# Kernel tuning notes

Measured on AMD Instinct MI355X. Metric: run time of the kernel, lower is better.

## Reference

```python
import jax, jax.numpy as jnp
import numpy as np

NU, NI, D, E = 50000, 100000, 128, 500000
UMAX, IMAX = 50, 50
SQRT_D = float(np.sqrt(D))


def seg_softmax(vals, seg, n):
    # numerically stable softmax over edges grouped by segment id (sparse row softmax)
    m = jax.ops.segment_max(vals, seg, num_segments=n)
    ex = jnp.exp(vals - m[seg])
    s = jax.ops.segment_sum(ex, seg, num_segments=n)
    return ex / s[seg]


def setup_inputs() -> dict:
    key = jax.random.key(0)
    ks = jax.random.split(key, 20)
    w = lambda k: jax.random.normal(k, (D, D), dtype=jnp.float32) * 0.05
    return {
        "u_emb": jax.random.normal(ks[0], (NU, D), dtype=jnp.float32),
        "i_emb": jax.random.normal(ks[1], (NI, D), dtype=jnp.float32),
        "edge_u": jax.random.randint(ks[2], (E,), 0, NU),
        "edge_i": jax.random.randint(ks[3], (E,), 0, NI),
        "rui": jax.random.randint(ks[4], (E,), 0, UMAX),
        "riu": jax.random.randint(ks[5], (E,), 0, IMAX),
        "last_u_items": jax.random.randint(ks[6], (NU,), 0, NI),
        "last_i_users": jax.random.randint(ks[7], (NU,), 0, NU),
        "W1": w(ks[8]), "W2": w(ks[9]), "W1b": w(ks[10]), "W2b": w(ks[11]),
        "W3": w(ks[12]), "W4": w(ks[13]),
        "pV": jax.random.normal(ks[14], (UMAX, D), dtype=jnp.float32),
        "pK": jax.random.normal(ks[15], (IMAX, D), dtype=jnp.float32),
        "last_user_table": jax.random.normal(ks[16], (NU, D), dtype=jnp.float32),
        "last_item_table": jax.random.normal(ks[17], (NI, D), dtype=jnp.float32),
    }


def reference(u_emb, i_emb, edge_u, edge_i, rui, riu, last_u_items, last_i_users,
              W1, W2, W1b, W2b, W3, W4, pV, pK, last_user_table, last_item_table):
    # nn.Linear: y = x @ W.T
    um = u_emb @ W2.T            # (NU, D) user messages
    im = i_emb @ W1.T            # (NI, D) item messages
    um_e = um[edge_u]            # (E, D) gathered per edge
    im_e = im[edge_i]            # (E, D)

    # ---- long term ----
    # dense e = um @ im.T masked to edges == per-edge dot products (same math)
    e_vals = jnp.sum(um_e * im_e, axis=-1)                     # (E,)
    pVui = pV[rui]                                             # (E, D)
    pKiu = pK[riu]                                             # (E, D)
    e_ui = e_vals + jnp.sum(um_e * pVui, axis=-1)
    e_iu = e_vals + jnp.sum(im_e * pKiu, axis=-1)
    alphas = seg_softmax(e_ui / SQRT_D, edge_u, NU)            # softmax over items per user
    betas = seg_softmax(e_iu / SQRT_D, edge_i, NI)             # softmax over users per item

    umb = u_emb @ W2b.T
    imb = i_emb @ W1b.T
    # pass_messages: out[row] = sum_e alpha_e * (messages[col_e] + p_e)
    hLu = jax.ops.segment_sum(alphas[:, None] * (imb[edge_i] + pKiu), edge_u, num_segments=NU)
    hLi = jax.ops.segment_sum(betas[:, None] * (umb[edge_u] + pVui), edge_i, num_segments=NI)

    # ---- short term ----
    li = last_item_table[last_u_items] @ W3.T                  # (NU, D)
    lu = last_user_table[last_i_users] @ W4.T                  # (NU, D)
    a_vals = jnp.sum(li[edge_u] * im_e, axis=-1)               # (E,)
    b_vals = jnp.sum(lu[edge_u] * im_e, axis=-1)               # (E,)
    alphas_s = seg_softmax(a_vals / SQRT_D, edge_u, NU)
    betas_s = seg_softmax(b_vals / SQRT_D, edge_i, NI)
    # p = ones -> messages + 1
    hSu = jax.ops.segment_sum(alphas_s[:, None] * (im_e + 1.0), edge_u, num_segments=NU)
    hSi = jax.ops.segment_sum(betas_s[:, None] * (um_e + 1.0), edge_i, num_segments=NI)

    return (hLu, hSu, hLi, hSi)
```

## Files before the change

kernel.cpp:

```cpp
#include <hip/hip_runtime.h>
#include <hip/hip_bf16.h>
#include <math.h>

#define D_ 128
#define INV_SQRT_D 0.08838834764831845f
#define SCAN_CH 16
#define SCAN_TILE (256 * SCAN_CH)

typedef __bf16 bf16x8 __attribute__((ext_vector_type(8)));
typedef float f32x4 __attribute__((ext_vector_type(4)));

struct W6 { const float* p[6]; };

__device__ __forceinline__ void unpack8(bf16x8 v, float* f) {
    const uint32_t* u = (const uint32_t*)&v;
#pragma unroll
    for (int i = 0; i < 4; i++) {
        uint32_t w = u[i];
        f[2 * i]     = __uint_as_float(w << 16);
        f[2 * i + 1] = __uint_as_float(w & 0xffff0000u);
    }
}

__global__ __launch_bounds__(256) void cvt_weights(W6 w, __bf16* __restrict__ out) {
    int idx = blockIdx.x * 256 + threadIdx.x;
    if (idx >= 6 * 16384) return;
    out[idx] = (__bf16)w.p[idx >> 14][idx & 16383];
}

__global__ __launch_bounds__(256) void cvt2(const float* __restrict__ a, const float* __restrict__ b,
                                            __bf16* __restrict__ oa, __bf16* __restrict__ ob, int n) {
    int idx = blockIdx.x * 256 + threadIdx.x;
    if (idx < n) { oa[idx] = (__bf16)a[idx]; ob[idx] = (__bf16)b[idx]; }
}

__global__ __launch_bounds__(256) void gemm_dual(const float* __restrict__ X,
                                                 const __bf16* __restrict__ WA,
                                                 const __bf16* __restrict__ WB,
                                                 __bf16* __restrict__ YA, int sA,
                                                 __bf16* __restrict__ YB, int sB, int rows) {
    int lane = threadIdx.x & 63;
    int wave = threadIdx.x >> 6;
    int row0 = blockIdx.x * 64 + wave * 16;
    if (row0 >= rows) return;
    int l16 = lane & 15, kh = lane >> 4;
    int ar = row0 + l16;
    int arc = ar < rows ? ar : rows - 1;
    const float* arow = X + (size_t)arc * D_;

    f32x4 accA[8] = {}, accB[8] = {};
#pragma unroll
    for (int k0 = 0; k0 < D_; k0 += 32) {
        int kk = k0 + kh * 8;
        float4 a0 = *(const float4*)(arow + kk);
        float4 a1 = *(const float4*)(arow + kk + 4);
        bf16x8 af;
        af[0] = (__bf16)a0.x; af[1] = (__bf16)a0.y; af[2] = (__bf16)a0.z; af[3] = (__bf16)a0.w;
        af[4] = (__bf16)a1.x; af[5] = (__bf16)a1.y; af[6] = (__bf16)a1.z; af[7] = (__bf16)a1.w;
#pragma unroll
        for (int cb = 0; cb < 8; cb++) {
            bf16x8 bfA = *(const bf16x8*)(WA + (size_t)(cb * 16 + l16) * D_ + kk);
            accA[cb] = __builtin_amdgcn_mfma_f32_16x16x32_bf16(af, bfA, accA[cb], 0, 0, 0);
            bf16x8 bfB = *(const bf16x8*)(WB + (size_t)(cb * 16 + l16) * D_ + kk);
            accB[cb] = __builtin_amdgcn_mfma_f32_16x16x32_bf16(af, bfB, accB[cb], 0, 0, 0);
        }
    }
#pragma unroll
    for (int cb = 0; cb < 8; cb++) {
#pragma unroll
        for (int j = 0; j < 4; j++) {
            int r = row0 + kh * 4 + j;
            if (r < rows) {
                YA[(size_t)r * sA + cb * 16 + l16] = (__bf16)accA[cb][j];
                YB[(size_t)r * sB + cb * 16 + l16] = (__bf16)accB[cb][j];
            }
        }
    }
}

__global__ __launch_bounds__(256) void gemm_lilu(const float* __restrict__ Xi, const int* __restrict__ gi_,
                                                 const float* __restrict__ Xu, const int* __restrict__ gu_,
                                                 const __bf16* __restrict__ Wli, const __bf16* __restrict__ Wlu,
                                                 __bf16* __restrict__ Yli, __bf16* __restrict__ Ylu, int rows) {
    int lane = threadIdx.x & 63;
    int wave = threadIdx.x >> 6;
    int row0 = blockIdx.x * 64 + wave * 16;
    if (row0 >= rows) return;
    int l16 = lane & 15, kh = lane >> 4;
    int ar = row0 + l16;
    int arc = ar < rows ? ar : rows - 1;
    const float* arowA = Xi + (size_t)gi_[arc] * D_;
    const float* arowB = Xu + (size_t)gu_[arc] * D_;

    f32x4 accA[8] = {}, accB[8] = {};
#pragma unroll
    for (int k0 = 0; k0 < D_; k0 += 32) {
        int kk = k0 + kh * 8;
        float4 a0 = *(const float4*)(arowA + kk);
        float4 a1 = *(const float4*)(arowA + kk + 4);
        float4 b0 = *(const float4*)(arowB + kk);
        float4 b1 = *(const float4*)(arowB + kk + 4);
        bf16x8 afA, afB;
        afA[0] = (__bf16)a0.x; afA[1] = (__bf16)a0.y; afA[2] = (__bf16)a0.z; afA[3] = (__bf16)a0.w;
        afA[4] = (__bf16)a1.x; afA[5] = (__bf16)a1.y; afA[6] = (__bf16)a1.z; afA[7] = (__bf16)a1.w;
        afB[0] = (__bf16)b0.x; afB[1] = (__bf16)b0.y; afB[2] = (__bf16)b0.z; afB[3] = (__bf16)b0.w;
        afB[4] = (__bf16)b1.x; afB[5] = (__bf16)b1.y; afB[6] = (__bf16)b1.z; afB[7] = (__bf16)b1.w;
#pragma unroll
        for (int cb = 0; cb < 8; cb++) {
            bf16x8 bfA = *(const bf16x8*)(Wli + (size_t)(cb * 16 + l16) * D_ + kk);
            accA[cb] = __builtin_amdgcn_mfma_f32_16x16x32_bf16(afA, bfA, accA[cb], 0, 0, 0);
            bf16x8 bfB = *(const bf16x8*)(Wlu + (size_t)(cb * 16 + l16) * D_ + kk);
            accB[cb] = __builtin_amdgcn_mfma_f32_16x16x32_bf16(afB, bfB, accB[cb], 0, 0, 0);
        }
    }
#pragma unroll
    for (int cb = 0; cb < 8; cb++) {
#pragma unroll
        for (int j = 0; j < 4; j++) {
            int r = row0 + kh * 4 + j;
            if (r < rows) {
                Yli[(size_t)r * D_ + cb * 16 + l16] = (__bf16)accA[cb][j];
                Ylu[(size_t)r * D_ + cb * 16 + l16] = (__bf16)accB[cb][j];
            }
        }
    }
}

__global__ __launch_bounds__(256) void gemm_pvk(const __bf16* __restrict__ Xb, int xstride,
                                                const __bf16* __restrict__ Pb,
                                                float* __restrict__ Y, int rows, int ncols) {
    int lane = threadIdx.x & 63;
    int wave = threadIdx.x >> 6;
    int row0 = blockIdx.x * 64 + wave * 16;
    if (row0 >= rows) return;
    int l16 = lane & 15, kh = lane >> 4;
    int ar = row0 + l16;
    int arc = ar < rows ? ar : rows - 1;
    const __bf16* arow = Xb + (size_t)arc * xstride;

    f32x4 acc[4] = {};
#pragma unroll
    for (int k0 = 0; k0 < D_; k0 += 32) {
        int kk = k0 + kh * 8;
        bf16x8 af = *(const bf16x8*)(arow + kk);
#pragma unroll
        for (int cb = 0; cb < 4; cb++) {
            int br = cb * 16 + l16;
            if (br >= ncols) br = ncols - 1;
            bf16x8 bf = *(const bf16x8*)(Pb + (size_t)br * D_ + kk);
            acc[cb] = __builtin_amdgcn_mfma_f32_16x16x32_bf16(af, bf, acc[cb], 0, 0, 0);
        }
    }
#pragma unroll
    for (int cb = 0; cb < 4; cb++) {
        int col = cb * 16 + l16;
        if (col >= ncols) continue;
#pragma unroll
        for (int j = 0; j < 4; j++) {
            int r = row0 + kh * 4 + j;
            if (r < rows) Y[(size_t)r * ncols + col] = acc[cb][j] * INV_SQRT_D;
        }
    }
}

__global__ __launch_bounds__(256) void hist2(const int* __restrict__ eu, const int* __restrict__ ei,
                                             int* __restrict__ cnt_all, int nu, int E) {
    int e = blockIdx.x * 256 + threadIdx.x;
    if (e < E) {
        atomicAdd(&cnt_all[eu[e]], 1);
        atomicAdd(&cnt_all[nu + ei[e]], 1);
    }
}

__global__ __launch_bounds__(256) void scan_phaseA(const int* __restrict__ cnt, int* __restrict__ part, int n) {
    __shared__ int wsum[4];
    int t = threadIdx.x, lane = t & 63, w = t >> 6;
    int i0 = blockIdx.x * SCAN_TILE + t * SCAN_CH;
    int tot = 0;
#pragma unroll
    for (int j = 0; j < SCAN_CH; j++) tot += (i0 + j < n) ? cnt[i0 + j] : 0;
#pragma unroll
    for (int d = 32; d; d >>= 1) tot += __shfl_xor(tot, d);
    if (lane == 0) wsum[w] = tot;
    __syncthreads();
    if (t == 0) part[blockIdx.x] = wsum[0] + wsum[1] + wsum[2] + wsum[3];
}

__global__ __launch_bounds__(1024) void scan_phaseB(int* __restrict__ part, int nb,
                                                    int* __restrict__ off, int n) {
    __shared__ int wsum[16];
    int t = threadIdx.x, lane = t & 63, w = t >> 6;
    int v = (t < nb) ? part[t] : 0;
    int x = v;
#pragma unroll
    for (int d = 1; d < 64; d <<= 1) {
        int y = __shfl_up(x, d);
        if (lane >= d) x += y;
    }
    if (lane == 63) wsum[w] = x;
    __syncthreads();
    int wbase = 0;
    for (int ww = 0; ww < w; ww++) wbase += wsum[ww];
    if (t < nb) part[t] = wbase + x - v;
    if (t == 1023) off[n] = wbase + x;
}

__global__ __launch_bounds__(256) void scan_phaseC(const int* __restrict__ cnt, const int* __restrict__ part,
                                                   int* __restrict__ off, int* __restrict__ pos, int n) {
    __shared__ int wsum[4];
    int t = threadIdx.x, lane = t & 63, w = t >> 6;
    int i0 = blockIdx.x * SCAN_TILE + t * SCAN_CH;
    int loc[SCAN_CH];
    int tot = 0;
#pragma unroll
    for (int j = 0; j < SCAN_CH; j++) {
        int v = (i0 + j < n) ? cnt[i0 + j] : 0;
        loc[j] = tot; tot += v;
    }
    int x = tot;
#pragma unroll
    for (int d = 1; d < 64; d <<= 1) {
        int y = __shfl_up(x, d);
        if (lane >= d) x += y;
    }
    if (lane == 63) wsum[w] = x;
    __syncthreads();
    int wbase = 0;
    for (int ww = 0; ww < w; ww++) wbase += wsum[ww];
    int excl = part[blockIdx.x] + wbase + x - tot;
#pragma unroll
    for (int j = 0; j < SCAN_CH; j++) {
        if (i0 + j < n) { off[i0 + j] = excl + loc[j]; pos[i0 + j] = excl + loc[j]; }
    }
}

__global__ __launch_bounds__(256) void scatter2(const int* __restrict__ eu, const int* __restrict__ ei,
                                                const int* __restrict__ rui, const int* __restrict__ riu,
                                                int* __restrict__ pos_all, int4* __restrict__ recs,
                                                int nu, int E) {
    int e = blockIdx.x * 256 + threadIdx.x;
    if (e < E) {
        int u = eu[e], it = ei[e], r1 = rui[e], r2 = riu[e];
        int pi = atomicAdd(&pos_all[nu + it], 1);
        int pu = atomicAdd(&pos_all[u], 1);
        recs[pu] = make_int4(it, r1, r2, pi);
        recs[pi] = make_int4(u, r1, r2, 0);
    }
}

__global__ __launch_bounds__(256) void user_fused(const int* __restrict__ off_all, const int4* __restrict__ recs,
                                                  const __bf16* __restrict__ i_rec,
                                                  const __bf16* __restrict__ u_rec,
                                                  const __bf16* __restrict__ li_t,
                                                  const __bf16* __restrict__ lu_t,
                                                  const __bf16* __restrict__ pKb,
                                                  const float* __restrict__ upv,
                                                  float2* __restrict__ mb_val,
                                                  float* __restrict__ hLu, float* __restrict__ hSu,
                                                  int nu, int umax) {
    int u = blockIdx.x * 4 + (threadIdx.x >> 6);
    if (u >= nu) return;
    int lane = threadIdx.x & 63;
    int g = lane >> 4, l16 = lane & 15;
    int off = off_all[u], n = off_all[u + 1] - off;
    if (n == 0) {
        if (lane < 16) {
            float4 z = make_float4(0.f, 0.f, 0.f, 0.f);
            ((float4*)(hLu + (size_t)u * D_ + l16 * 8))[0] = z;
            ((float4*)(hLu + (size_t)u * D_ + l16 * 8))[1] = z;
            ((float4*)(hSu + (size_t)u * D_ + l16 * 8))[0] = z;
            ((float4*)(hSu + (size_t)u * D_ + l16 * 8))[1] = z;
        }
        return;
    }
    float um8[8], li8[8], lu8[8];
    unpack8(((const bf16x8*)(u_rec + (size_t)u * 256))[l16], um8);
    unpack8(((const bf16x8*)(li_t + (size_t)u * D_))[l16], li8);
    unpack8(((const bf16x8*)(lu_t + (size_t)u * D_))[l16], lu8);
#pragma unroll
    for (int j = 0; j < 8; j++) { um8[j] *= INV_SQRT_D; li8[j] *= INV_SQRT_D; lu8[j] *= INV_SQRT_D; }
    const float* upv_row = upv + (size_t)u * umax;

    float s1 = 0.f, s2 = 0.f, a1[8] = {}, a2[8] = {};
    for (int i = g; i < n; i += 8) {
        int4 ra = recs[off + i];
        bool hb = (i + 4) < n;
        int4 rb = recs[off + (hb ? i + 4 : i)];
        const __bf16* pa = i_rec + (size_t)ra.x * 256;
        const __bf16* pb = i_rec + (size_t)rb.x * 256;
        bf16x8 vimA = ((const bf16x8*)pa)[l16];
        bf16x8 vmbA = ((const bf16x8*)(pa + 128))[l16];
        bf16x8 vpkA = ((const bf16x8*)(pKb + (size_t)ra.z * D_))[l16];
        bf16x8 vimB = ((const bf16x8*)pb)[l16];
        bf16x8 vmbB = ((const bf16x8*)(pb + 128))[l16];
        bf16x8 vpkB = ((const bf16x8*)(pKb + (size_t)rb.z * D_))[l16];
        float fimA[8], fmbA[8], fpkA[8], fimB[8], fmbB[8], fpkB[8];
        unpack8(vimA, fimA); unpack8(vmbA, fmbA); unpack8(vpkA, fpkA);
        unpack8(vimB, fimB); unpack8(vmbB, fmbB); unpack8(vpkB, fpkB);
        float d1a = 0.f, d2a = 0.f, d3a = 0.f, d1b = 0.f, d2b = 0.f, d3b = 0.f;
#pragma unroll
        for (int j = 0; j < 8; j++) {
            d1a = fmaf(um8[j], fimA[j], d1a);
            d2a = fmaf(li8[j], fimA[j], d2a);
            d3a = fmaf(lu8[j], fimA[j], d3a);
            d1b = fmaf(um8[j], fimB[j], d1b);
            d2b = fmaf(li8[j], fimB[j], d2b);
            d3b = fmaf(lu8[j], fimB[j], d3b);
        }
#pragma unroll
        for (int d = 1; d < 16; d <<= 1) {
            d1a += __shfl_xor(d1a, d); d2a += __shfl_xor(d2a, d); d3a += __shfl_xor(d3a, d);
            d1b += __shfl_xor(d1b, d); d2b += __shfl_xor(d2b, d); d3b += __shfl_xor(d3b, d);
        }
        if (l16 == 0) {
            mb_val[ra.w] = make_float2(d1a, d3a);
            if (hb) mb_val[rb.w] = make_float2(d1b, d3b);
        }
        float w1a = __expf(d1a + upv_row[ra.y]);
        float w2a = __expf(d2a);
        float w1b = hb ? __expf(d1b + upv_row[rb.y]) : 0.f;
        float w2b = hb ? __expf(d2b) : 0.f;
        s1 += w1a + w1b; s2 += w2a + w2b;
#pragma unroll
        for (int j = 0; j < 8; j++) {
            a1[j] = fmaf(w1a, fmbA[j] + fpkA[j], fmaf(w1b, fmbB[j] + fpkB[j], a1[j]));
            a2[j] = fmaf(w2a, fimA[j], fmaf(w2b, fimB[j], a2[j]));
        }
    }
#pragma unroll
    for (int d = 16; d < 64; d <<= 1) {
        s1 += __shfl_xor(s1, d); s2 += __shfl_xor(s2, d);
#pragma unroll
        for (int j = 0; j < 8; j++) {
            a1[j] += __shfl_xor(a1[j], d);
            a2[j] += __shfl_xor(a2[j], d);
        }
    }
    if (lane < 16) {
        float inv1 = 1.f / s1, inv2 = 1.f / s2;
        ((float4*)(hLu + (size_t)u * D_ + l16 * 8))[0] = make_float4(a1[0]*inv1, a1[1]*inv1, a1[2]*inv1, a1[3]*inv1);
        ((float4*)(hLu + (size_t)u * D_ + l16 * 8))[1] = make_float4(a1[4]*inv1, a1[5]*inv1, a1[6]*inv1, a1[7]*inv1);
        ((float4*)(hSu + (size_t)u * D_ + l16 * 8))[0] = make_float4(a2[0]*inv2+1.f, a2[1]*inv2+1.f, a2[2]*inv2+1.f, a2[3]*inv2+1.f);
        ((float4*)(hSu + (size_t)u * D_ + l16 * 8))[1] = make_float4(a2[4]*inv2+1.f, a2[5]*inv2+1.f, a2[6]*inv2+1.f, a2[7]*inv2+1.f);
    }
}

__global__ __launch_bounds__(256) void item_fused(const int* __restrict__ off_all, const int4* __restrict__ recs,
                                                  const __bf16* __restrict__ u_rec,
                                                  const __bf16* __restrict__ pVb,
                                                  const float* __restrict__ ipk,
                                                  const float2* __restrict__ mb_val,
                                                  float* __restrict__ hLi, float* __restrict__ hSi,
                                                  int nu, int ni, int imax) {
    int it = blockIdx.x * 4 + (threadIdx.x >> 6);
    if (it >= ni) return;
    int lane = threadIdx.x & 63;
    int g = lane >> 4, l16 = lane & 15;
    int off = off_all[nu + it], n = off_all[nu + it + 1] - off;
    if (n == 0) {
        if (lane < 16) {
            float4 z = make_float4(0.f, 0.f, 0.f, 0.f);
            ((float4*)(hLi + (size_t)it * D_ + l16 * 8))[0] = z;
            ((float4*)(hLi + (size_t)it * D_ + l16 * 8))[1] = z;
            ((float4*)(hSi + (size_t)it * D_ + l16 * 8))[0] = z;
            ((float4*)(hSi + (size_t)it * D_ + l16 * 8))[1] = z;
        }
        return;
    }
    const float* ipk_row = ipk + (size_t)it * imax;

    float s1 = 0.f, s2 = 0.f, a1[8] = {}, a2[8] = {};
    for (int i = g; i < n; i += 8) {
        int4 ra = recs[off + i];
        bool hb = (i + 4) < n;
        int4 rb = recs[off + (hb ? i + 4 : i)];
        float2 ma = mb_val[off + i];
        float2 mbv = hb ? mb_val[off + i + 4] : make_float2(0.f, 0.f);
        const __bf16* pa = u_rec + (size_t)ra.x * 256;
        const __bf16* pb = u_rec + (size_t)rb.x * 256;
        bf16x8 vumA  = ((const bf16x8*)pa)[l16];
        bf16x8 vmbA  = ((const bf16x8*)(pa + 128))[l16];
        bf16x8 vpvA  = ((const bf16x8*)(pVb + (size_t)ra.y * D_))[l16];
        bf16x8 vumB  = ((const bf16x8*)pb)[l16];
        bf16x8 vmbB  = ((const bf16x8*)(pb + 128))[l16];
        bf16x8 vpvB  = ((const bf16x8*)(pVb + (size_t)rb.y * D_))[l16];
        float fumA[8], fmbA[8], fpvA[8], fumB[8], fmbB[8], fpvB[8];
        unpack8(vumA, fumA); unpack8(vmbA, fmbA); unpack8(vpvA, fpvA);
        unpack8(vumB, fumB); unpack8(vmbB, fmbB); unpack8(vpvB, fpvB);
        float w1a = __expf(ma.x + ipk_row[ra.z]);
        float w2a = __expf(ma.y);
        float w1b = hb ? __expf(mbv.x + ipk_row[rb.z]) : 0.f;
        float w2b = hb ? __expf(mbv.y) : 0.f;
        s1 += w1a + w1b; s2 += w2a + w2b;
#pragma unroll
        for (int j = 0; j < 8; j++) {
            a1[j] = fmaf(w1a, fmbA[j] + fpvA[j], fmaf(w1b, fmbB[j] + fpvB[j], a1[j]));
            a2[j] = fmaf(w2a, fumA[j], fmaf(w2b, fumB[j], a2[j]));
        }
    }
#pragma unroll
    for (int d = 16; d < 64; d <<= 1) {
        s1 += __shfl_xor(s1, d); s2 += __shfl_xor(s2, d);
#pragma unroll
        for (int j = 0; j < 8; j++) {
            a1[j] += __shfl_xor(a1[j], d);
            a2[j] += __shfl_xor(a2[j], d);
        }
    }
    if (lane < 16) {
        float inv1 = 1.f / s1, inv2 = 1.f / s2;
        ((float4*)(hLi + (size_t)it * D_ + l16 * 8))[0] = make_float4(a1[0]*inv1, a1[1]*inv1, a1[2]*inv1, a1[3]*inv1);
        ((float4*)(hLi + (size_t)it * D_ + l16 * 8))[1] = make_float4(a1[4]*inv1, a1[5]*inv1, a1[6]*inv1, a1[7]*inv1);
        ((float4*)(hSi + (size_t)it * D_ + l16 * 8))[0] = make_float4(a2[0]*inv2+1.f, a2[1]*inv2+1.f, a2[2]*inv2+1.f, a2[3]*inv2+1.f);
        ((float4*)(hSi + (size_t)it * D_ + l16 * 8))[1] = make_float4(a2[4]*inv2+1.f, a2[5]*inv2+1.f, a2[6]*inv2+1.f, a2[7]*inv2+1.f);
    }
}

extern "C" void kernel_launch(void* const* d_in, const int* in_sizes, int n_in,
                              void* d_out, int out_size, void* d_ws, size_t ws_size,
                              hipStream_t stream) {
    (void)n_in; (void)out_size; (void)ws_size;
    const float* u_emb = (const float*)d_in[0];
    const float* i_emb = (const float*)d_in[1];
    const int* edge_u = (const int*)d_in[2];
    const int* edge_i = (const int*)d_in[3];
    const int* rui = (const int*)d_in[4];
    const int* riu = (const int*)d_in[5];
    const int* last_u_items = (const int*)d_in[6];
    const int* last_i_users = (const int*)d_in[7];
    const float* W1  = (const float*)d_in[8];
    const float* W2  = (const float*)d_in[9];
    const float* W1b = (const float*)d_in[10];
    const float* W2b = (const float*)d_in[11];
    const float* W3  = (const float*)d_in[12];
    const float* W4  = (const float*)d_in[13];
    const float* pV  = (const float*)d_in[14];
    const float* pK  = (const float*)d_in[15];
    const float* last_user_table = (const float*)d_in[16];
    const float* last_item_table = (const float*)d_in[17];

    const int NU = in_sizes[0] / D_;
    const int NI = in_sizes[1] / D_;
    const int E  = in_sizes[2];
    const int UMAXr = in_sizes[14] / D_;
    const int IMAXr = in_sizes[15] / D_;
    const int NSEG = NU + NI;

    size_t cur = 0;
    auto alloc = [&](size_t bytes) -> void* {
        void* p = (char*)d_ws + cur;
        cur += (bytes + 255) & ~(size_t)255;
        return p;
    };

    __bf16* Wb    = (__bf16*)alloc(6 * 16384 * sizeof(__bf16));
    __bf16* pVb   = (__bf16*)alloc((size_t)UMAXr * D_ * 2);
    __bf16* pKb   = (__bf16*)alloc((size_t)IMAXr * D_ * 2);
    __bf16* i_rec = (__bf16*)alloc((size_t)NI * 256 * 2);
    __bf16* u_rec = (__bf16*)alloc((size_t)NU * 256 * 2);
    __bf16* li_bf = (__bf16*)alloc((size_t)NU * D_ * 2);
    __bf16* lu_bf = (__bf16*)alloc((size_t)NU * D_ * 2);
    float* upv    = (float*)alloc((size_t)NU * UMAXr * 4);
    float* ipk    = (float*)alloc((size_t)NI * IMAXr * 4);
    float2* mb_val = (float2*)alloc((size_t)2 * E * 8);
    int4* recs    = (int4*)alloc((size_t)2 * E * 16);
    int* cnt_all  = (int*)alloc((size_t)NSEG * 4);
    int* off_all  = (int*)alloc((size_t)(NSEG + 1) * 4);
    int* pos_all  = (int*)alloc((size_t)NSEG * 4);
    int* parts    = (int*)alloc(1024 * 4);

    float* out = (float*)d_out;
    float* hLu = out;
    float* hSu = out + (size_t)NU * D_;
    float* hLi = out + (size_t)2 * NU * D_;
    float* hSi = out + (size_t)2 * NU * D_ + (size_t)NI * D_;

    W6 w6;
    w6.p[0] = W1; w6.p[1] = W2; w6.p[2] = W1b; w6.p[3] = W2b; w6.p[4] = W3; w6.p[5] = W4;
    cvt_weights<<<(6 * 16384 + 255) / 256, 256, 0, stream>>>(w6, Wb);
    cvt2<<<(UMAXr * D_ + 255) / 256, 256, 0, stream>>>(pV, pK, pVb, pKb, UMAXr * D_);

    hipMemsetAsync(cnt_all, 0, (size_t)NSEG * 4, stream);
    hist2<<<(E + 255) / 256, 256, 0, stream>>>(edge_u, edge_i, cnt_all, NU, E);
    int nb = (NSEG + SCAN_TILE - 1) / SCAN_TILE;
    scan_phaseA<<<nb, 256, 0, stream>>>(cnt_all, parts, NSEG);
    scan_phaseB<<<1, 1024, 0, stream>>>(parts, nb, off_all, NSEG);
    scan_phaseC<<<nb, 256, 0, stream>>>(cnt_all, parts, off_all, pos_all, NSEG);
    scatter2<<<(E + 255) / 256, 256, 0, stream>>>(edge_u, edge_i, rui, riu, pos_all, recs, NU, E);

    int gu = (NU + 63) / 64, gi = (NI + 63) / 64;
    gemm_dual<<<gi, 256, 0, stream>>>(i_emb, Wb + 0 * 16384, Wb + 2 * 16384,
                                      i_rec + 0, 256, i_rec + 128, 256, NI);
    gemm_dual<<<gu, 256, 0, stream>>>(u_emb, Wb + 1 * 16384, Wb + 3 * 16384,
                                      u_rec + 0, 256, u_rec + 128, 256, NU);
    gemm_lilu<<<gu, 256, 0, stream>>>(last_item_table, last_u_items, last_user_table, last_i_users,
                                      Wb + 4 * 16384, Wb + 5 * 16384, li_bf, lu_bf, NU);

    gemm_pvk<<<gu, 256, 0, stream>>>(u_rec, 256, pVb, upv, NU, UMAXr);
    gemm_pvk<<<gi, 256, 0, stream>>>(i_rec, 256, pKb, ipk, NI, IMAXr);

    user_fused<<<(NU + 3) / 4, 256, 0, stream>>>(off_all, recs, i_rec, u_rec, li_bf, lu_bf,
                                                 pKb, upv, mb_val, hLu, hSu, NU, UMAXr);
    item_fused<<<(NI + 3) / 4, 256, 0, stream>>>(off_all, recs, u_rec, pVb, ipk, mb_val,
                                                 hLi, hSi, NU, NI, IMAXr);
}
```

Before: 489.3 us.

## Reassociate projections: gather raw bf16 embeddings, apply weights after aggregation

Folds the weight matrices algebraically. Combined matrices such as W1ᵀW2, W1ᵀW3, W1ᵀW4 and pV·W2 are precomputed so that per-edge scores use raw bf16 embeddings instead of projected messages. The segment aggregation now runs on raw embeddings, and the W1b/W2b and W1/W2 projections are applied once per node afterwards in a new finish GEMM, which also adds the positional term and the +1 offset. This halves the bytes gathered per edge (128 instead of 256 bf16 per record) and removes the item/user message GEMMs before the passes. In exchange it adds an embedding conversion pass, bf16 intermediate buffers and two post-GEMMs, and changes where rounding happens.

```diff
diff --git a/kernel.cpp b/kernel.cpp
--- a/kernel.cpp
+++ b/kernel.cpp
@@ -10,7 +10,7 @@
 typedef __bf16 bf16x8 __attribute__((ext_vector_type(8)));
 typedef float f32x4 __attribute__((ext_vector_type(4)));
 
-struct W6 { const float* p[6]; };
+struct W4p { const float* p[4]; };
 
 __device__ __forceinline__ void unpack8(bf16x8 v, float* f) {
     const uint32_t* u = (const uint32_t*)&v;
@@ -22,9 +22,16 @@
     }
 }
 
-__global__ __launch_bounds__(256) void cvt_weights(W6 w, __bf16* __restrict__ out) {
+__device__ __forceinline__ bf16x8 pack8(const float* f, float s) {
+    bf16x8 r;
+#pragma unroll
+    for (int j = 0; j < 8; j++) r[j] = (__bf16)(f[j] * s);
+    return r;
+}
+
+__global__ __launch_bounds__(256) void cvt_weights4(W4p w, __bf16* __restrict__ out) {
     int idx = blockIdx.x * 256 + threadIdx.x;
-    if (idx >= 6 * 16384) return;
+    if (idx >= 4 * 16384) return;
     out[idx] = (__bf16)w.p[idx >> 14][idx & 16383];
 }
 
@@ -34,11 +41,64 @@
     if (idx < n) { oa[idx] = (__bf16)a[idx]; ob[idx] = (__bf16)b[idx]; }
 }
 
-__global__ __launch_bounds__(256) void gemm_dual(const float* __restrict__ X,
-                                                 const __bf16* __restrict__ WA,
-                                                 const __bf16* __restrict__ WB,
-                                                 __bf16* __restrict__ YA, int sA,
-                                                 __bf16* __restrict__ YB, int sB, int rows) {
+__global__ __launch_bounds__(256) void cvt_emb(const float* __restrict__ u, const float* __restrict__ i,
+                                               __bf16* __restrict__ ub, __bf16* __restrict__ ib,
+                                               size_t nue, size_t nie) {
+    size_t idx4 = ((size_t)blockIdx.x * 256 + threadIdx.x) * 4;
+    if (idx4 < nue) {
+        float4 v = *(const float4*)(u + idx4);
+        ub[idx4] = (__bf16)v.x; ub[idx4+1] = (__bf16)v.y; ub[idx4+2] = (__bf16)v.z; ub[idx4+3] = (__bf16)v.w;
+    } else if (idx4 < nue + nie) {
+        size_t j = idx4 - nue;
+        float4 v = *(const float4*)(i + j);
+        ib[j] = (__bf16)v.x; ib[j+1] = (__bf16)v.y; ib[j+2] = (__bf16)v.z; ib[j+3] = (__bf16)v.w;
+    }
+}
+
+__global__ __launch_bounds__(128) void prep_mats(const float* __restrict__ W1, const float* __restrict__ W2,
+                                                 const float* __restrict__ W3, const float* __restrict__ W4,
+                                                 const float* __restrict__ pV, const float* __restrict__ pK,
+                                                 __bf16* __restrict__ M2t, __bf16* __restrict__ M3t,
+                                                 __bf16* __restrict__ M4t,
+                                                 __bf16* __restrict__ pVW2, __bf16* __restrict__ pKW1,
+                                                 int umax, int imax) {
+    __shared__ float sh[256];
+    int b = blockIdx.x, t = threadIdx.x;
+    if (b < 128) {
+        sh[t] = W1[t * 128 + b];
+        __syncthreads();
+        float m2 = 0.f, m3 = 0.f, m4 = 0.f;
+        for (int k = 0; k < 128; k++) {
+            float w = sh[k];
+            m2 = fmaf(w, W2[k * 128 + t], m2);
+            m3 = fmaf(w, W3[k * 128 + t], m3);
+            m4 = fmaf(w, W4[k * 128 + t], m4);
+        }
+        M2t[b * 128 + t] = (__bf16)(m2 * INV_SQRT_D);
+        M3t[b * 128 + t] = (__bf16)(m3 * INV_SQRT_D);
+        M4t[b * 128 + t] = (__bf16)(m4 * INV_SQRT_D);
+    } else {
+        int r = b - 128;
+        if (r < umax) sh[t] = pV[r * 128 + t];
+        if (r < imax) sh[128 + t] = pK[r * 128 + t];
+        __syncthreads();
+        float q = 0.f, qk = 0.f;
+        for (int a = 0; a < 128; a++) {
+            if (r < umax) q  = fmaf(sh[a], W2[a * 128 + t], q);
+            if (r < imax) qk = fmaf(sh[128 + a], W1[a * 128 + t], qk);
+        }
+        if (r < umax) pVW2[r * 128 + t] = (__bf16)(q * INV_SQRT_D);
+        if (r < imax) pKW1[r * 128 + t] = (__bf16)(qk * INV_SQRT_D);
+    }
+}
+
+__global__ __launch_bounds__(256) void user_vecs(const float* __restrict__ u_emb,
+                                                 const float* __restrict__ lit_tab, const int* __restrict__ g_li,
+                                                 const float* __restrict__ lut_tab, const int* __restrict__ g_lu,
+                                                 const __bf16* __restrict__ M2t, const __bf16* __restrict__ M3t,
+                                                 const __bf16* __restrict__ M4t,
+                                                 __bf16* __restrict__ um_t, __bf16* __restrict__ li_t,
+                                                 __bf16* __restrict__ lu_t, int rows) {
     int lane = threadIdx.x & 63;
     int wave = threadIdx.x >> 6;
     int row0 = blockIdx.x * 64 + wave * 16;
@@ -46,23 +106,32 @@
     int l16 = lane & 15, kh = lane >> 4;
     int ar = row0 + l16;
     int arc = ar < rows ? ar : rows - 1;
-    const float* arow = X + (size_t)arc * D_;
-
-    f32x4 accA[8] = {}, accB[8] = {};
+    const float* rA = u_emb + (size_t)arc * D_;
+    const float* rB = lit_tab + (size_t)g_li[arc] * D_;
+    const float* rC = lut_tab + (size_t)g_lu[arc] * D_;
+
+    f32x4 aA[8] = {}, aB[8] = {}, aC[8] = {};
 #pragma unroll
     for (int k0 = 0; k0 < D_; k0 += 32) {
         int kk = k0 + kh * 8;
-        float4 a0 = *(const float4*)(arow + kk);
-        float4 a1 = *(const float4*)(arow + kk + 4);
-        bf16x8 af;
-        af[0] = (__bf16)a0.x; af[1] = (__bf16)a0.y; af[2] = (__bf16)a0.z; af[3] = (__bf16)a0.w;
-        af[4] = (__bf16)a1.x; af[5] = (__bf16)a1.y; af[6] = (__bf16)a1.z; af[7] = (__bf16)a1.w;
+        float4 a0 = *(const float4*)(rA + kk), a1 = *(const float4*)(rA + kk + 4);
+        float4 b0 = *(const float4*)(rB + kk), b1 = *(const float4*)(rB + kk + 4);
+        float4 c0 = *(const float4*)(rC + kk), c1 = *(const float4*)(rC + kk + 4);
+        bf16x8 fA, fB, fC;
+        fA[0]=(__bf16)a0.x; fA[1]=(__bf16)a0.y; fA[2]=(__bf16)a0.z; fA[3]=(__bf16)a0.w;
+        fA[4]=(__bf16)a1.x; fA[5]=(__bf16)a1.y; fA[6]=(__bf16)a1.z; fA[7]=(__bf16)a1.w;
+        fB[0]=(__bf16)b0.x; fB[1]=(__bf16)b0.y; fB[2]=(__bf16)b0.z; fB[3]=(__bf16)b0.w;
+        fB[4]=(__bf16)b1.x; fB[5]=(__bf16)b1.y; fB[6]=(__bf16)b1.z; fB[7]=(__bf16)b1.w;
+        fC[0]=(__bf16)c0.x; fC[1]=(__bf16)c0.y; fC[2]=(__bf16)c0.z; fC[3]=(__bf16)c0.w;
+        fC[4]=(__bf16)c1.x; fC[5]=(__bf16)c1.y; fC[6]=(__bf16)c1.z; fC[7]=(__bf16)c1.w;
 #pragma unroll
         for (int cb = 0; cb < 8; cb++) {
-            bf16x8 bfA = *(const bf16x8*)(WA + (size_t)(cb * 16 + l16) * D_ + kk);
-            accA[cb] = __builtin_amdgcn_mfma_f32_16x16x32_bf16(af, bfA, accA[cb], 0, 0, 0);
-            bf16x8 bfB = *(const bf16x8*)(WB + (size_t)(cb * 16 + l16) * D_ + kk);
-            accB[cb] = __builtin_amdgcn_mfma_f32_16x16x32_bf16(af, bfB, accB[cb], 0, 0, 0);
+            bf16x8 w2 = *(const bf16x8*)(M2t + (size_t)(cb * 16 + l16) * D_ + kk);
+            aA[cb] = __builtin_amdgcn_mfma_f32_16x16x32_bf16(fA, w2, aA[cb], 0, 0, 0);
+            bf16x8 w3 = *(const bf16x8*)(M3t + (size_t)(cb * 16 + l16) * D_ + kk);
+            aB[cb] = __builtin_amdgcn_mfma_f32_16x16x32_bf16(fB, w3, aB[cb], 0, 0, 0);
+            bf16x8 w4 = *(const bf16x8*)(M4t + (size_t)(cb * 16 + l16) * D_ + kk);
+            aC[cb] = __builtin_amdgcn_mfma_f32_16x16x32_bf16(fC, w4, aC[cb], 0, 0, 0);
         }
     }
 #pragma unroll
@@ -71,62 +140,15 @@
         for (int j = 0; j < 4; j++) {
             int r = row0 + kh * 4 + j;
             if (r < rows) {
-                YA[(size_t)r * sA + cb * 16 + l16] = (__bf16)accA[cb][j];
-                YB[(size_t)r * sB + cb * 16 + l16] = (__bf16)accB[cb][j];
+                um_t[(size_t)r * D_ + cb * 16 + l16] = (__bf16)aA[cb][j];
+                li_t[(size_t)r * D_ + cb * 16 + l16] = (__bf16)aB[cb][j];
+                lu_t[(size_t)r * D_ + cb * 16 + l16] = (__bf16)aC[cb][j];
             }
         }
     }
 }
 
-__global__ __launch_bounds__(256) void gemm_lilu(const float* __restrict__ Xi, const int* __restrict__ gi_,
-                                                 const float* __restrict__ Xu, const int* __restrict__ gu_,
-                                                 const __bf16* __restrict__ Wli, const __bf16* __restrict__ Wlu,
-                                                 __bf16* __restrict__ Yli, __bf16* __restrict__ Ylu, int rows) {
-    int lane = threadIdx.x & 63;
-    int wave = threadIdx.x >> 6;
-    int row0 = blockIdx.x * 64 + wave * 16;
-    if (row0 >= rows) return;
-    int l16 = lane & 15, kh = lane >> 4;
-    int ar = row0 + l16;
-    int arc = ar < rows ? ar : rows - 1;
-    const float* arowA = Xi + (size_t)gi_[arc] * D_;
-    const float* arowB = Xu + (size_t)gu_[arc] * D_;
-
-    f32x4 accA[8] = {}, accB[8] = {};
-#pragma unroll
-    for (int k0 = 0; k0 < D_; k0 += 32) {
-        int kk = k0 + kh * 8;
-        float4 a0 = *(const float4*)(arowA + kk);
-        float4 a1 = *(const float4*)(arowA + kk + 4);
-        float4 b0 = *(const float4*)(arowB + kk);
-        float4 b1 = *(const float4*)(arowB + kk + 4);
-        bf16x8 afA, afB;
-        afA[0] = (__bf16)a0.x; afA[1] = (__bf16)a0.y; afA[2] = (__bf16)a0.z; afA[3] = (__bf16)a0.w;
-        afA[4] = (__bf16)a1.x; afA[5] = (__bf16)a1.y; afA[6] = (__bf16)a1.z; afA[7] = (__bf16)a1.w;
-        afB[0] = (__bf16)b0.x; afB[1] = (__bf16)b0.y; afB[2] = (__bf16)b0.z; afB[3] = (__bf16)b0.w;
-        afB[4] = (__bf16)b1.x; afB[5] = (__bf16)b1.y; afB[6] = (__bf16)b1.z; afB[7] = (__bf16)b1.w;
-#pragma unroll
-        for (int cb = 0; cb < 8; cb++) {
-            bf16x8 bfA = *(const bf16x8*)(Wli + (size_t)(cb * 16 + l16) * D_ + kk);
-            accA[cb] = __builtin_amdgcn_mfma_f32_16x16x32_bf16(afA, bfA, accA[cb], 0, 0, 0);
-            bf16x8 bfB = *(const bf16x8*)(Wlu + (size_t)(cb * 16 + l16) * D_ + kk);
-            accB[cb] = __builtin_amdgcn_mfma_f32_16x16x32_bf16(afB, bfB, accB[cb], 0, 0, 0);
-        }
-    }
-#pragma unroll
-    for (int cb = 0; cb < 8; cb++) {
-#pragma unroll
-        for (int j = 0; j < 4; j++) {
-            int r = row0 + kh * 4 + j;
-            if (r < rows) {
-                Yli[(size_t)r * D_ + cb * 16 + l16] = (__bf16)accA[cb][j];
-                Ylu[(size_t)r * D_ + cb * 16 + l16] = (__bf16)accB[cb][j];
-            }
-        }
-    }
-}
-
-__global__ __launch_bounds__(256) void gemm_pvk(const __bf16* __restrict__ Xb, int xstride,
+__global__ __launch_bounds__(256) void gemm_pvk(const __bf16* __restrict__ Xb,
                                                 const __bf16* __restrict__ Pb,
                                                 float* __restrict__ Y, int rows, int ncols) {
     int lane = threadIdx.x & 63;
@@ -136,7 +158,7 @@
     int l16 = lane & 15, kh = lane >> 4;
     int ar = row0 + l16;
     int arc = ar < rows ? ar : rows - 1;
-    const __bf16* arow = Xb + (size_t)arc * xstride;
+    const __bf16* arow = Xb + (size_t)arc * D_;
 
     f32x4 acc[4] = {};
 #pragma unroll
@@ -158,7 +180,7 @@
 #pragma unroll
         for (int j = 0; j < 4; j++) {
             int r = row0 + kh * 4 + j;
-            if (r < rows) Y[(size_t)r * ncols + col] = acc[cb][j] * INV_SQRT_D;
+            if (r < rows) Y[(size_t)r * ncols + col] = acc[cb][j];
         }
     }
 }
@@ -248,16 +270,16 @@
     }
 }
 
-__global__ __launch_bounds__(256) void user_fused(const int* __restrict__ off_all, const int4* __restrict__ recs,
-                                                  const __bf16* __restrict__ i_rec,
-                                                  const __bf16* __restrict__ u_rec,
-                                                  const __bf16* __restrict__ li_t,
-                                                  const __bf16* __restrict__ lu_t,
-                                                  const __bf16* __restrict__ pKb,
-                                                  const float* __restrict__ upv,
-                                                  float2* __restrict__ mb_val,
-                                                  float* __restrict__ hLu, float* __restrict__ hSu,
-                                                  int nu, int umax) {
+__global__ __launch_bounds__(256) void user_pass(const int* __restrict__ off_all, const int4* __restrict__ recs,
+                                                 const __bf16* __restrict__ ib_emb,
+                                                 const __bf16* __restrict__ um_t,
+                                                 const __bf16* __restrict__ li_t,
+                                                 const __bf16* __restrict__ lu_t,
+                                                 const __bf16* __restrict__ pKb,
+                                                 const float* __restrict__ upv,
+                                                 float2* __restrict__ mb_val,
+                                                 __bf16* __restrict__ A1n, __bf16* __restrict__ PKn,
+                                                 __bf16* __restrict__ A2n, int nu, int umax) {
     int u = blockIdx.x * 4 + (threadIdx.x >> 6);
     if (u >= nu) return;
     int lane = threadIdx.x & 63;
@@ -265,47 +287,40 @@
     int off = off_all[u], n = off_all[u + 1] - off;
     if (n == 0) {
         if (lane < 16) {
-            float4 z = make_float4(0.f, 0.f, 0.f, 0.f);
-            ((float4*)(hLu + (size_t)u * D_ + l16 * 8))[0] = z;
-            ((float4*)(hLu + (size_t)u * D_ + l16 * 8))[1] = z;
-            ((float4*)(hSu + (size_t)u * D_ + l16 * 8))[0] = z;
-            ((float4*)(hSu + (size_t)u * D_ + l16 * 8))[1] = z;
+            bf16x8 z = {};
+            *(bf16x8*)(A1n + (size_t)u * D_ + l16 * 8) = z;
+            *(bf16x8*)(PKn + (size_t)u * D_ + l16 * 8) = z;
+            *(bf16x8*)(A2n + (size_t)u * D_ + l16 * 8) = z;
         }
         return;
     }
     float um8[8], li8[8], lu8[8];
-    unpack8(((const bf16x8*)(u_rec + (size_t)u * 256))[l16], um8);
+    unpack8(((const bf16x8*)(um_t + (size_t)u * D_))[l16], um8);
     unpack8(((const bf16x8*)(li_t + (size_t)u * D_))[l16], li8);
     unpack8(((const bf16x8*)(lu_t + (size_t)u * D_))[l16], lu8);
-#pragma unroll
-    for (int j = 0; j < 8; j++) { um8[j] *= INV_SQRT_D; li8[j] *= INV_SQRT_D; lu8[j] *= INV_SQRT_D; }
     const float* upv_row = upv + (size_t)u * umax;
 
-    float s1 = 0.f, s2 = 0.f, a1[8] = {}, a2[8] = {};
+    float s1 = 0.f, s2 = 0.f, a1[8] = {}, apk[8] = {}, a2[8] = {};
     for (int i = g; i < n; i += 8) {
         int4 ra = recs[off + i];
         bool hb = (i + 4) < n;
         int4 rb = recs[off + (hb ? i + 4 : i)];
-        const __bf16* pa = i_rec + (size_t)ra.x * 256;
-        const __bf16* pb = i_rec + (size_t)rb.x * 256;
-        bf16x8 vimA = ((const bf16x8*)pa)[l16];
-        bf16x8 vmbA = ((const bf16x8*)(pa + 128))[l16];
+        bf16x8 vieA = ((const bf16x8*)(ib_emb + (size_t)ra.x * D_))[l16];
         bf16x8 vpkA = ((const bf16x8*)(pKb + (size_t)ra.z * D_))[l16];
-        bf16x8 vimB = ((const bf16x8*)pb)[l16];
-        bf16x8 vmbB = ((const bf16x8*)(pb + 128))[l16];
+        bf16x8 vieB = ((const bf16x8*)(ib_emb + (size_t)rb.x * D_))[l16];
         bf16x8 vpkB = ((const bf16x8*)(pKb + (size_t)rb.z * D_))[l16];
-        float fimA[8], fmbA[8], fpkA[8], fimB[8], fmbB[8], fpkB[8];
-        unpack8(vimA, fimA); unpack8(vmbA, fmbA); unpack8(vpkA, fpkA);
-        unpack8(vimB, fimB); unpack8(vmbB, fmbB); unpack8(vpkB, fpkB);
+        float fieA[8], fpkA[8], fieB[8], fpkB[8];
+        unpack8(vieA, fieA); unpack8(vpkA, fpkA);
+        unpack8(vieB, fieB); unpack8(vpkB, fpkB);
         float d1a = 0.f, d2a = 0.f, d3a = 0.f, d1b = 0.f, d2b = 0.f, d3b = 0.f;
 #pragma unroll
         for (int j = 0; j < 8; j++) {
-            d1a = fmaf(um8[j], fimA[j], d1a);
-            d2a = fmaf(li8[j], fimA[j], d2a);
-            d3a = fmaf(lu8[j], fimA[j], d3a);
-            d1b = fmaf(um8[j], fimB[j], d1b);
-            d2b = fmaf(li8[j], fimB[j], d2b);
-            d3b = fmaf(lu8[j], fimB[j], d3b);
+            d1a = fmaf(um8[j], fieA[j], d1a);
+            d2a = fmaf(li8[j], fieA[j], d2a);
+            d3a = fmaf(lu8[j], fieA[j], d3a);
+            d1b = fmaf(um8[j], fieB[j], d1b);
+            d2b = fmaf(li8[j], fieB[j], d2b);
+            d3b = fmaf(lu8[j], fieB[j], d3b);
         }
 #pragma unroll
         for (int d = 1; d < 16; d <<= 1) {
@@ -323,8 +338,9 @@
         s1 += w1a + w1b; s2 += w2a + w2b;
 #pragma unroll
         for (int j = 0; j < 8; j++) {
-            a1[j] = fmaf(w1a, fmbA[j] + fpkA[j], fmaf(w1b, fmbB[j] + fpkB[j], a1[j]));
-            a2[j] = fmaf(w2a, fimA[j], fmaf(w2b, fimB[j], a2[j]));
+            a1[j]  = fmaf(w1a, fieA[j], fmaf(w1b, fieB[j], a1[j]));
+            apk[j] = fmaf(w1a, fpkA[j], fmaf(w1b, fpkB[j], apk[j]));
+            a2[j]  = fmaf(w2a, fieA[j], fmaf(w2b, fieB[j], a2[j]));
         }
     }
 #pragma unroll
@@ -332,26 +348,26 @@
         s1 += __shfl_xor(s1, d); s2 += __shfl_xor(s2, d);
 #pragma unroll
         for (int j = 0; j < 8; j++) {
-            a1[j] += __shfl_xor(a1[j], d);
-            a2[j] += __shfl_xor(a2[j], d);
+            a1[j]  += __shfl_xor(a1[j], d);
+            apk[j] += __shfl_xor(apk[j], d);
+            a2[j]  += __shfl_xor(a2[j], d);
         }
     }
     if (lane < 16) {
         float inv1 = 1.f / s1, inv2 = 1.f / s2;
-        ((float4*)(hLu + (size_t)u * D_ + l16 * 8))[0] = make_float4(a1[0]*inv1, a1[1]*inv1, a1[2]*inv1, a1[3]*inv1);
-        ((float4*)(hLu + (size_t)u * D_ + l16 * 8))[1] = make_float4(a1[4]*inv1, a1[5]*inv1, a1[6]*inv1, a1[7]*inv1);
-        ((float4*)(hSu + (size_t)u * D_ + l16 * 8))[0] = make_float4(a2[0]*inv2+1.f, a2[1]*inv2+1.f, a2[2]*inv2+1.f, a2[3]*inv2+1.f);
-        ((float4*)(hSu + (size_t)u * D_ + l16 * 8))[1] = make_float4(a2[4]*inv2+1.f, a2[5]*inv2+1.f, a2[6]*inv2+1.f, a2[7]*inv2+1.f);
-    }
-}
-
-__global__ __launch_bounds__(256) void item_fused(const int* __restrict__ off_all, const int4* __restrict__ recs,
-                                                  const __bf16* __restrict__ u_rec,
-                                                  const __bf16* __restrict__ pVb,
-                                                  const float* __restrict__ ipk,
-                                                  const float2* __restrict__ mb_val,
-                                                  float* __restrict__ hLi, float* __restrict__ hSi,
-                                                  int nu, int ni, int imax) {
+        *(bf16x8*)(A1n + (size_t)u * D_ + l16 * 8) = pack8(a1, inv1);
+        *(bf16x8*)(PKn + (size_t)u * D_ + l16 * 8) = pack8(apk, inv1);
+        *(bf16x8*)(A2n + (size_t)u * D_ + l16 * 8) = pack8(a2, inv2);
+    }
+}
+
+__global__ __launch_bounds__(256) void item_pass(const int* __restrict__ off_all, const int4* __restrict__ recs,
+                                                 const __bf16* __restrict__ ub_emb,
+                                                 const __bf16* __restrict__ pVb,
+                                                 const float* __restrict__ ipk,
+                                                 const float2* __restrict__ mb_val,
+                                                 __bf16* __restrict__ B1n, __bf16* __restrict__ PVn,
+                                                 __bf16* __restrict__ B2n, int nu, int ni, int imax) {
     int it = blockIdx.x * 4 + (threadIdx.x >> 6);
     if (it >= ni) return;
     int lane = threadIdx.x & 63;
@@ -359,34 +375,29 @@
     int off = off_all[nu + it], n = off_all[nu + it + 1] - off;
     if (n == 0) {
         if (lane < 16) {
-            float4 z = make_float4(0.f, 0.f, 0.f, 0.f);
-            ((float4*)(hLi + (size_t)it * D_ + l16 * 8))[0] = z;
-            ((float4*)(hLi + (size_t)it * D_ + l16 * 8))[1] = z;
-            ((float4*)(hSi + (size_t)it * D_ + l16 * 8))[0] = z;
-            ((float4*)(hSi + (size_t)it * D_ + l16 * 8))[1] = z;
+            bf16x8 z = {};
+            *(bf16x8*)(B1n + (size_t)it * D_ + l16 * 8) = z;
+            *(bf16x8*)(PVn + (size_t)it * D_ + l16 * 8) = z;
+            *(bf16x8*)(B2n + (size_t)it * D_ + l16 * 8) = z;
         }
         return;
     }
     const float* ipk_row = ipk + (size_t)it * imax;
 
-    float s1 = 0.f, s2 = 0.f, a1[8] = {}, a2[8] = {};
+    float s1 = 0.f, s2 = 0.f, b1[8] = {}, bpv[8] = {}, b2[8] = {};
     for (int i = g; i < n; i += 8) {
         int4 ra = recs[off + i];
         bool hb = (i + 4) < n;
         int4 rb = recs[off + (hb ? i + 4 : i)];
         float2 ma = mb_val[off + i];
         float2 mbv = hb ? mb_val[off + i + 4] : make_float2(0.f, 0.f);
-        const __bf16* pa = u_rec + (size_t)ra.x * 256;
-        const __bf16* pb = u_rec + (size_t)rb.x * 256;
-        bf16x8 vumA  = ((const bf16x8*)pa)[l16];
-        bf16x8 vmbA  = ((const bf16x8*)(pa + 128))[l16];
-        bf16x8 vpvA  = ((const bf16x8*)(pVb + (size_t)ra.y * D_))[l16];
-        bf16x8 vumB  = ((const bf16x8*)pb)[l16];
-        bf16x8 vmbB  = ((const bf16x8*)(pb + 128))[l16];
-        bf16x8 vpvB  = ((const bf16x8*)(pVb + (size_t)rb.y * D_))[l16];
-        float fumA[8], fmbA[8], fpvA[8], fumB[8], fmbB[8], fpvB[8];
-        unpack8(vumA, fumA); unpack8(vmbA, fmbA); unpack8(vpvA, fpvA);
-        unpack8(vumB, fumB); unpack8(vmbB, fmbB); unpack8(vpvB, fpvB);
+        bf16x8 vueA = ((const bf16x8*)(ub_emb + (size_t)ra.x * D_))[l16];
+        bf16x8 vpvA = ((const bf16x8*)(pVb + (size_t)ra.y * D_))[l16];
+        bf16x8 vueB = ((const bf16x8*)(ub_emb + (size_t)rb.x * D_))[l16];
+        bf16x8 vpvB = ((const bf16x8*)(pVb + (size_t)rb.y * D_))[l16];
+        float fueA[8], fpvA[8], fueB[8], fpvB[8];
+        unpack8(vueA, fueA); unpack8(vpvA, fpvA);
+        unpack8(vueB, fueB); unpack8(vpvB, fpvB);
         float w1a = __expf(ma.x + ipk_row[ra.z]);
         float w2a = __expf(ma.y);
         float w1b = hb ? __expf(mbv.x + ipk_row[rb.z]) : 0.f;
@@ -394,8 +405,9 @@
         s1 += w1a + w1b; s2 += w2a + w2b;
 #pragma unroll
         for (int j = 0; j < 8; j++) {
-            a1[j] = fmaf(w1a, fmbA[j] + fpvA[j], fmaf(w1b, fmbB[j] + fpvB[j], a1[j]));
-            a2[j] = fmaf(w2a, fumA[j], fmaf(w2b, fumB[j], a2[j]));
+            b1[j]  = fmaf(w1a, fueA[j], fmaf(w1b, fueB[j], b1[j]));
+            bpv[j] = fmaf(w1a, fpvA[j], fmaf(w1b, fpvB[j], bpv[j]));
+            b2[j]  = fmaf(w2a, fueA[j], fmaf(w2b, fueB[j], b2[j]));
         }
     }
 #pragma unroll
@@ -403,16 +415,61 @@
         s1 += __shfl_xor(s1, d); s2 += __shfl_xor(s2, d);
 #pragma unroll
         for (int j = 0; j < 8; j++) {
-            a1[j] += __shfl_xor(a1[j], d);
-            a2[j] += __shfl_xor(a2[j], d);
+            b1[j]  += __shfl_xor(b1[j], d);
+            bpv[j] += __shfl_xor(bpv[j], d);
+            b2[j]  += __shfl_xor(b2[j], d);
         }
     }
     if (lane < 16) {
         float inv1 = 1.f / s1, inv2 = 1.f / s2;
-        ((float4*)(hLi + (size_t)it * D_ + l16 * 8))[0] = make_float4(a1[0]*inv1, a1[1]*inv1, a1[2]*inv1, a1[3]*inv1);
-        ((float4*)(hLi + (size_t)it * D_ + l16 * 8))[1] = make_float4(a1[4]*inv1, a1[5]*inv1, a1[6]*inv1, a1[7]*inv1);
-        ((float4*)(hSi + (size_t)it * D_ + l16 * 8))[0] = make_float4(a2[0]*inv2+1.f, a2[1]*inv2+1.f, a2[2]*inv2+1.f, a2[3]*inv2+1.f);
-        ((float4*)(hSi + (size_t)it * D_ + l16 * 8))[1] = make_float4(a2[4]*inv2+1.f, a2[5]*inv2+1.f, a2[6]*inv2+1.f, a2[7]*inv2+1.f);
+        *(bf16x8*)(B1n + (size_t)it * D_ + l16 * 8) = pack8(b1, inv1);
+        *(bf16x8*)(PVn + (size_t)it * D_ + l16 * 8) = pack8(bpv, inv1);
+        *(bf16x8*)(B2n + (size_t)it * D_ + l16 * 8) = pack8(b2, inv2);
+    }
+}
+
+__global__ __launch_bounds__(256) void finish2(const __bf16* __restrict__ A1, const __bf16* __restrict__ WA,
+                                               const __bf16* __restrict__ side,
+                                               const __bf16* __restrict__ A2, const __bf16* __restrict__ WB,
+                                               float* __restrict__ out1, float* __restrict__ out2,
+                                               const int* __restrict__ offseg, int rows) {
+    int lane = threadIdx.x & 63;
+    int wave = threadIdx.x >> 6;
+    int row0 = blockIdx.x * 64 + wave * 16;
+    if (row0 >= rows) return;
+    int l16 = lane & 15, kh = lane >> 4;
+    int ar = row0 + l16;
+    int arc = ar < rows ? ar : rows - 1;
+    const __bf16* r1 = A1 + (size_t)arc * D_;
+    const __bf16* r2 = A2 + (size_t)arc * D_;
+
+    f32x4 acc1[8] = {}, acc2[8] = {};
+#pragma unroll
+    for (int k0 = 0; k0 < D_; k0 += 32) {
+        int kk = k0 + kh * 8;
+        bf16x8 f1 = *(const bf16x8*)(r1 + kk);
+        bf16x8 f2 = *(const bf16x8*)(r2 + kk);
+#pragma unroll
+        for (int cb = 0; cb < 8; cb++) {
+            bf16x8 wa = *(const bf16x8*)(WA + (size_t)(cb * 16 + l16) * D_ + kk);
+            acc1[cb] = __builtin_amdgcn_mfma_f32_16x16x32_bf16(f1, wa, acc1[cb], 0, 0, 0);
+            bf16x8 wb = *(const bf16x8*)(WB + (size_t)(cb * 16 + l16) * D_ + kk);
+            acc2[cb] = __builtin_amdgcn_mfma_f32_16x16x32_bf16(f2, wb, acc2[cb], 0, 0, 0);
+        }
+    }
+#pragma unroll
+    for (int cb = 0; cb < 8; cb++) {
+#pragma unroll
+        for (int j = 0; j < 4; j++) {
+            int r = row0 + kh * 4 + j;
+            if (r < rows) {
+                int c = cb * 16 + l16;
+                float sv = (float)side[(size_t)r * D_ + c];
+                out1[(size_t)r * D_ + c] = acc1[cb][j] + sv;
+                float one = (offseg[r + 1] - offseg[r]) > 0 ? 1.f : 0.f;
+                out2[(size_t)r * D_ + c] = acc2[cb][j] + one;
+            }
+        }
     }
 }
 
@@ -453,15 +510,27 @@
         return p;
     };
 
-    __bf16* Wb    = (__bf16*)alloc(6 * 16384 * sizeof(__bf16));
+    __bf16* Wb4   = (__bf16*)alloc(4 * 16384 * 2);
+    __bf16* M2t   = (__bf16*)alloc(16384 * 2);
+    __bf16* M3t   = (__bf16*)alloc(16384 * 2);
+    __bf16* M4t   = (__bf16*)alloc(16384 * 2);
+    __bf16* pVW2  = (__bf16*)alloc((size_t)UMAXr * D_ * 2);
+    __bf16* pKW1  = (__bf16*)alloc((size_t)IMAXr * D_ * 2);
     __bf16* pVb   = (__bf16*)alloc((size_t)UMAXr * D_ * 2);
     __bf16* pKb   = (__bf16*)alloc((size_t)IMAXr * D_ * 2);
-    __bf16* i_rec = (__bf16*)alloc((size_t)NI * 256 * 2);
-    __bf16* u_rec = (__bf16*)alloc((size_t)NU * 256 * 2);
-    __bf16* li_bf = (__bf16*)alloc((size_t)NU * D_ * 2);
-    __bf16* lu_bf = (__bf16*)alloc((size_t)NU * D_ * 2);
+    __bf16* ub_emb = (__bf16*)alloc((size_t)NU * D_ * 2);
+    __bf16* ib_emb = (__bf16*)alloc((size_t)NI * D_ * 2);
+    __bf16* um_t  = (__bf16*)alloc((size_t)NU * D_ * 2);
+    __bf16* li_t  = (__bf16*)alloc((size_t)NU * D_ * 2);
+    __bf16* lu_t  = (__bf16*)alloc((size_t)NU * D_ * 2);
     float* upv    = (float*)alloc((size_t)NU * UMAXr * 4);
     float* ipk    = (float*)alloc((size_t)NI * IMAXr * 4);
+    __bf16* A1n   = (__bf16*)alloc((size_t)NU * D_ * 2);
+    __bf16* PKn   = (__bf16*)alloc((size_t)NU * D_ * 2);
+    __bf16* A2n   = (__bf16*)alloc((size_t)NU * D_ * 2);
+    __bf16* B1n   = (__bf16*)alloc((size_t)NI * D_ * 2);
+    __bf16* PVn   = (__bf16*)alloc((size_t)NI * D_ * 2);
+    __bf16* B2n   = (__bf16*)alloc((size_t)NI * D_ * 2);
     float2* mb_val = (float2*)alloc((size_t)2 * E * 8);
     int4* recs    = (int4*)alloc((size_t)2 * E * 16);
     int* cnt_all  = (int*)alloc((size_t)NSEG * 4);
@@ -475,10 +544,13 @@
     float* hLi = out + (size_t)2 * NU * D_;
     float* hSi = out + (size_t)2 * NU * D_ + (size_t)NI * D_;
 
-    W6 w6;
-    w6.p[0] = W1; w6.p[1] = W2; w6.p[2] = W1b; w6.p[3] = W2b; w6.p[4] = W3; w6.p[5] = W4;
-    cvt_weights<<<(6 * 16384 + 255) / 256, 256, 0, stream>>>(w6, Wb);
+    W4p w4; w4.p[0] = W1; w4.p[1] = W2; w4.p[2] = W1b; w4.p[3] = W2b;
+    cvt_weights4<<<(4 * 16384 + 255) / 256, 256, 0, stream>>>(w4, Wb4);
+    prep_mats<<<128 + (UMAXr > IMAXr ? UMAXr : IMAXr), 128, 0, stream>>>(W1, W2, W3, W4, pV, pK,
+                                                                         M2t, M3t, M4t, pVW2, pKW1, UMAXr, IMAXr);
     cvt2<<<(UMAXr * D_ + 255) / 256, 256, 0, stream>>>(pV, pK, pVb, pKb, UMAXr * D_);
+    size_t nue = (size_t)NU * D_, nie = (size_t)NI * D_;
+    cvt_emb<<<(int)(((nue + nie) / 4 + 255) / 256), 256, 0, stream>>>(u_emb, i_emb, ub_emb, ib_emb, nue, nie);
 
     hipMemsetAsync(cnt_all, 0, (size_t)NSEG * 4, stream);
     hist2<<<(E + 255) / 256, 256, 0, stream>>>(edge_u, edge_i, cnt_all, NU, E);
@@ -489,18 +561,18 @@
     scatter2<<<(E + 255) / 256, 256, 0, stream>>>(edge_u, edge_i, rui, riu, pos_all, recs, NU, E);
 
     int gu = (NU + 63) / 64, gi = (NI + 63) / 64;
-    gemm_dual<<<gi, 256, 0, stream>>>(i_emb, Wb + 0 * 16384, Wb + 2 * 16384,
-                                      i_rec + 0, 256, i_rec + 128, 256, NI);
-    gemm_dual<<<gu, 256, 0, stream>>>(u_emb, Wb + 1 * 16384, Wb + 3 * 16384,
-                                      u_rec + 0, 256, u_rec + 128, 256, NU);
-    gemm_lilu<<<gu, 256, 0, stream>>>(last_item_table, last_u_items, last_user_table, last_i_users,
-                                      Wb + 4 * 16384, Wb + 5 * 16384, li_bf, lu_bf, NU);
-
-    gemm_pvk<<<gu, 256, 0, stream>>>(u_rec, 256, pVb, upv, NU, UMAXr);
-    gemm_pvk<<<gi, 256, 0, stream>>>(i_rec, 256, pKb, ipk, NI, IMAXr);
-
-    user_fused<<<(NU + 3) / 4, 256, 0, stream>>>(off_all, recs, i_rec, u_rec, li_bf, lu_bf,
-                                                 pKb, upv, mb_val, hLu, hSu, NU, UMAXr);
-    item_fused<<<(NI + 3) / 4, 256, 0, stream>>>(off_all, recs, u_rec, pVb, ipk, mb_val,
-                                                 hLi, hSi, NU, NI, IMAXr);
-}
+    user_vecs<<<gu, 256, 0, stream>>>(u_emb, last_item_table, last_u_items, last_user_table, last_i_users,
+                                      M2t, M3t, M4t, um_t, li_t, lu_t, NU);
+    gemm_pvk<<<gu, 256, 0, stream>>>(ub_emb, pVW2, upv, NU, UMAXr);
+    gemm_pvk<<<gi, 256, 0, stream>>>(ib_emb, pKW1, ipk, NI, IMAXr);
+
+    user_pass<<<(NU + 3) / 4, 256, 0, stream>>>(off_all, recs, ib_emb, um_t, li_t, lu_t,
+                                                pKb, upv, mb_val, A1n, PKn, A2n, NU, UMAXr);
+    item_pass<<<(NI + 3) / 4, 256, 0, stream>>>(off_all, recs, ub_emb, pVb, ipk, mb_val,
+                                                B1n, PVn, B2n, NU, NI, IMAXr);
+
+    finish2<<<gu, 256, 0, stream>>>(A1n, Wb4 + 2 * 16384, PKn, A2n, Wb4 + 0 * 16384,
+                                    hLu, hSu, off_all, NU);
+    finish2<<<gi, 256, 0, stream>>>(B1n, Wb4 + 3 * 16384, PVn, B2n, Wb4 + 1 * 16384,
+                                    hLi, hSi, off_all + NU, NI);
+}
```

New measurement: 596.8 us. +22.0%, slower.
